# Performance work log

Hardware: AMD Instinct MI355X
Metric: run time of the kernel (lower is better)

The kernel has to match this reference:

```python
import jax, jax.numpy as jnp
import numpy as np

B, D, H = 64, 1024, 1024  # batch, input_dim, hidden_dim


def setup_inputs() -> dict:
    key = jax.random.key(0)
    k_x, k_inW, k_hW = jax.random.split(key, 3)
    # Observed binary inputs in {0,1} -> Bernoulli-sample branch never taken.
    x = jax.random.randint(k_x, (B, D), 0, 2).astype(jnp.float32)
    # Kaiming-normal init: std = sqrt(2 / fan_in)
    in_W = jax.random.normal(k_inW, (H, D), dtype=jnp.float32) * np.float32(np.sqrt(2.0 / D))
    in_b = jnp.zeros((H,), dtype=jnp.float32)
    h_W = jax.random.normal(k_hW, (D, H), dtype=jnp.float32) * np.float32(np.sqrt(2.0 / H))
    h_b = jnp.zeros((D,), dtype=jnp.float32)
    return {"x": x, "in_W": in_W, "in_b": in_b, "h_W": h_W, "h_b": h_b}


def reference(x, in_W, in_b, h_W, h_b):
    # NADE recurrence: a_i = in_b + sum_{j<i} x_j * in_W[:, j]
    # Vectorized via exclusive cumulative sum of rank-1 contributions.
    contrib = jnp.einsum("bd,hd->bdh", x, in_W)          # [B, D, H]
    cum = jnp.cumsum(contrib, axis=1)
    a = jnp.concatenate([jnp.zeros_like(cum[:, :1]), cum[:, :-1]], axis=1) + in_b  # exclusive
    h = jax.nn.relu(a)                                    # [B, D, H]
    # p_i = sigmoid(relu(a_i) . h_W[i] + h_b[i])
    p_hat = jax.nn.sigmoid(jnp.einsum("bdh,dh->bd", h, h_W) + h_b)  # [B, D]
    return p_hat
```

## Files before the change

kernel.cpp:

```cpp
#include <hip/hip_runtime.h>
#include <hip/hip_bf16.h>

#define B 64
#define D 1024
#define H 1024
#define C 32
#define L (D / C)
#define BG 4
#define NBG (B / BG)
#define HQ 4
#define HP (H / HQ)

__device__ __forceinline__ float dpp_xor1(float v) {
    int i = __builtin_bit_cast(int, v);
    i = __builtin_amdgcn_mov_dpp(i, 0xB1, 0xF, 0xF, true);
    return __builtin_bit_cast(float, i);
}
__device__ __forceinline__ float dpp_xor2(float v) {
    int i = __builtin_bit_cast(int, v);
    i = __builtin_amdgcn_mov_dpp(i, 0x4E, 0xF, 0xF, true);
    return __builtin_bit_cast(float, i);
}

__global__ void k_transpose(const float* __restrict__ in, float* __restrict__ out) {
    __shared__ float tile[32][33];
    int bx = blockIdx.x * 32;
    int by = blockIdx.y * 32;
    int tx = threadIdx.x;
    int ty = threadIdx.y;
    #pragma unroll
    for (int r = 0; r < 32; r += 8)
        tile[ty + r][tx] = in[(by + ty + r) * D + (bx + tx)];
    __syncthreads();
    #pragma unroll
    for (int r = 0; r < 32; r += 8)
        out[(bx + ty + r) * H + (by + tx)] = tile[tx][ty + r];
}

__global__ void __launch_bounds__(256)
k_chunk_sums(const float* __restrict__ x,
             const float* __restrict__ Wt,
             float* __restrict__ S) {
    int blk = blockIdx.x;
    int bg  = blk >> 7;
    int chq = blk & 127;
    int c   = chq >> 2;
    int hq  = chq & 3;
    int b0  = bg * BG;
    int tid = threadIdx.x;
    int h   = hq * HP + tid;

    __shared__ float4 xs4[L];
    if (tid < L) {
        int i = c * L + tid;
        xs4[tid] = make_float4(x[(size_t)b0 * D + i],
                               x[(size_t)(b0 + 1) * D + i],
                               x[(size_t)(b0 + 2) * D + i],
                               x[(size_t)(b0 + 3) * D + i]);
    }
    __syncthreads();

    float acc0 = 0.f, acc1 = 0.f, acc2 = 0.f, acc3 = 0.f;
    #pragma unroll
    for (int j = 0; j < L; ++j) {
        float w = Wt[(size_t)(c * L + j) * H + h];
        float4 xf = xs4[j];
        acc0 = fmaf(xf.x, w, acc0);
        acc1 = fmaf(xf.y, w, acc1);
        acc2 = fmaf(xf.z, w, acc2);
        acc3 = fmaf(xf.w, w, acc3);
    }
    S[((size_t)b0 * C + c) * H + h]       = acc0;
    S[((size_t)(b0 + 1) * C + c) * H + h] = acc1;
    S[((size_t)(b0 + 2) * C + c) * H + h] = acc2;
    S[((size_t)(b0 + 3) * C + c) * H + h] = acc3;
}

__global__ void k_scan(float* __restrict__ S) {
    int tid = blockIdx.x * blockDim.x + threadIdx.x;
    if (tid >= B * H) return;
    int b = tid / H;
    int h = tid % H;
    float run = 0.f;
    #pragma unroll
    for (int c = 0; c < C; ++c) {
        int idx = (b * C + c) * H + h;
        float v = S[idx];
        S[idx] = run;
        run += v;
    }
}

__global__ void __launch_bounds__(256)
k_nade_main(const float* __restrict__ x,
            const float* __restrict__ Wt,
            const float* __restrict__ in_b,
            const float* __restrict__ h_W,
            const float* __restrict__ h_b,
            const float* __restrict__ P,
            float* __restrict__ Q) {
    int blk = blockIdx.x;
    int bg  = blk >> 7;
    int chq = blk & 127;
    int c   = chq >> 2;
    int hq  = chq & 3;
    int b0  = bg * BG;
    int tid = threadIdx.x;
    int h   = hq * HP + tid;
    int lane = tid & 63;
    int wv = tid >> 6;
    int ph = lane & 3;

    __shared__ float4 xs4[L];
    if (tid < L) {
        int i = c * L + tid;
        xs4[tid] = make_float4(x[(size_t)b0 * D + i],
                               x[(size_t)(b0 + 1) * D + i],
                               x[(size_t)(b0 + 2) * D + i],
                               x[(size_t)(b0 + 3) * D + i]);
    }

    float ib = in_b[h];
    float a0 = P[((size_t)b0 * C + c) * H + h] + ib;
    float a1 = P[((size_t)(b0 + 1) * C + c) * H + h] + ib;
    float a2 = P[((size_t)(b0 + 2) * C + c) * H + h] + ib;
    float a3 = P[((size_t)(b0 + 3) * C + c) * H + h] + ib;

    __syncthreads();

    bool k0 = (ph == 0), k1 = (ph == 1), k2 = (ph == 2), k3 = (ph == 3);

    float pr0[8], pr1[8], pr2[8], pr3[8];
    #pragma unroll
    for (int s = 0; s < 8; ++s) { pr0[s] = 0.f; pr1[s] = 0.f; pr2[s] = 0.f; pr3[s] = 0.f; }

    #pragma unroll
    for (int il = 0; il < L; ++il) {
        int i = c * L + il;
        float w  = h_W[(size_t)i * H + h];
        float wt = Wt[(size_t)i * H + h];
        float4 xf = xs4[il];
        int s = il >> 2;
        bool keep = (il & 3) == 0 ? k0 : ((il & 3) == 1 ? k1 : ((il & 3) == 2 ? k2 : k3));

        float p0 = fmaxf(a0, 0.f) * w;
        float t0 = p0 + dpp_xor1(p0); t0 = t0 + dpp_xor2(t0);
        pr0[s] = keep ? t0 : pr0[s];
        a0 = fmaf(xf.x, wt, a0);

        float p1 = fmaxf(a1, 0.f) * w;
        float t1 = p1 + dpp_xor1(p1); t1 = t1 + dpp_xor2(t1);
        pr1[s] = keep ? t1 : pr1[s];
        a1 = fmaf(xf.y, wt, a1);

        float p2 = fmaxf(a2, 0.f) * w;
        float t2 = p2 + dpp_xor1(p2); t2 = t2 + dpp_xor2(t2);
        pr2[s] = keep ? t2 : pr2[s];
        a2 = fmaf(xf.z, wt, a2);

        float p3 = fmaxf(a3, 0.f) * w;
        float t3 = p3 + dpp_xor1(p3); t3 = t3 + dpp_xor2(t3);
        pr3[s] = keep ? t3 : pr3[s];
        a3 = fmaf(xf.w, wt, a3);
    }

    #pragma unroll
    for (int s = 0; s < 8; ++s) {
        float v;
        v = pr0[s];
        v += __shfl_xor(v, 4, 64); v += __shfl_xor(v, 8, 64);
        v += __shfl_xor(v, 16, 64); v += __shfl_xor(v, 32, 64);
        pr0[s] = v;
        v = pr1[s];
        v += __shfl_xor(v, 4, 64); v += __shfl_xor(v, 8, 64);
        v += __shfl_xor(v, 16, 64); v += __shfl_xor(v, 32, 64);
        pr1[s] = v;
        v = pr2[s];
        v += __shfl_xor(v, 4, 64); v += __shfl_xor(v, 8, 64);
        v += __shfl_xor(v, 16, 64); v += __shfl_xor(v, 32, 64);
        pr2[s] = v;
        v = pr3[s];
        v += __shfl_xor(v, 4, 64); v += __shfl_xor(v, 8, 64);
        v += __shfl_xor(v, 16, 64); v += __shfl_xor(v, 32, 64);
        pr3[s] = v;
    }

    __shared__ float red[4][BG][L];
    if (lane < 4) {
        #pragma unroll
        for (int s = 0; s < 8; ++s) {
            red[wv][0][s * 4 + lane] = pr0[s];
            red[wv][1][s * 4 + lane] = pr1[s];
            red[wv][2][s * 4 + lane] = pr2[s];
            red[wv][3][s * 4 + lane] = pr3[s];
        }
    }
    __syncthreads();

    if (tid < BG * L) {
        int b = tid >> 5;
        int il = tid & 31;
        float t = red[0][b][il] + red[1][b][il] + red[2][b][il] + red[3][b][il];
        Q[((size_t)hq * B + (b0 + b)) * D + c * L + il] = t;
    }
}

__global__ void __launch_bounds__(256)
k_combine(const float* __restrict__ Q,
          const float* __restrict__ h_b,
          float* __restrict__ out) {
    int idx = blockIdx.x * blockDim.x + threadIdx.x;
    if (idx >= B * D) return;
    int d = idx & (D - 1);
    float t = Q[idx] + Q[(size_t)B * D + idx] + Q[2 * (size_t)B * D + idx]
            + Q[3 * (size_t)B * D + idx] + h_b[d];
    out[idx] = 1.0f / (1.0f + expf(-t));
}

extern "C" void kernel_launch(void* const* d_in, const int* in_sizes, int n_in,
                              void* d_out, int out_size, void* d_ws, size_t ws_size,
                              hipStream_t stream) {
    const float* x    = (const float*)d_in[0];
    const float* in_W = (const float*)d_in[1];
    const float* in_b = (const float*)d_in[2];
    const float* h_W  = (const float*)d_in[3];
    const float* h_b  = (const float*)d_in[4];
    float* out = (float*)d_out;

    float* Wt = (float*)d_ws;
    float* S  = Wt + (size_t)D * H;
    float* Q  = S + (size_t)B * C * H;

    dim3 tb(32, 8);
    dim3 tg(D / 32, H / 32);
    k_transpose<<<tg, tb, 0, stream>>>(in_W, Wt);

    k_chunk_sums<<<NBG * C * HQ, 256, 0, stream>>>(x, Wt, S);

    k_scan<<<(B * H + 255) / 256, 256, 0, stream>>>(S);

    k_nade_main<<<NBG * C * HQ, 256, 0, stream>>>(x, Wt, in_b, h_W, h_b, S, Q);

    k_combine<<<(B * D + 255) / 256, 256, 0, stream>>>(Q, h_b, out);
}
```

Baseline: 41.20 us.

## Drop transpose and scan kernels; read in_W rows directly and prefix-sum inline

Removes the in_W transpose kernel: each thread now loads its own contiguous 32-float row segment of in_W with float4 loads into registers, in both the chunk-sum and main kernels. Removes the separate scan kernel by having the main kernel sum the preceding chunk sums itself, which costs a variable-length loop of up to 31 iterations per thread. Adds a launch_bounds occupancy hint. Two kernel launches and a full transpose pass go away, in exchange for uncoalesced strided row loads (each lane reads a different row) and redundant prefix work per block.

```diff
diff --git a/kernel.cpp b/kernel.cpp
--- a/kernel.cpp
+++ b/kernel.cpp
@@ -22,24 +22,9 @@
     return __builtin_bit_cast(float, i);
 }
 
-__global__ void k_transpose(const float* __restrict__ in, float* __restrict__ out) {
-    __shared__ float tile[32][33];
-    int bx = blockIdx.x * 32;
-    int by = blockIdx.y * 32;
-    int tx = threadIdx.x;
-    int ty = threadIdx.y;
-    #pragma unroll
-    for (int r = 0; r < 32; r += 8)
-        tile[ty + r][tx] = in[(by + ty + r) * D + (bx + tx)];
-    __syncthreads();
-    #pragma unroll
-    for (int r = 0; r < 32; r += 8)
-        out[(bx + ty + r) * H + (by + tx)] = tile[tx][ty + r];
-}
-
 __global__ void __launch_bounds__(256)
 k_chunk_sums(const float* __restrict__ x,
-             const float* __restrict__ Wt,
+             const float* __restrict__ in_W,
              float* __restrict__ S) {
     int blk = blockIdx.x;
     int bg  = blk >> 7;
@@ -58,13 +43,21 @@
                                x[(size_t)(b0 + 2) * D + i],
                                x[(size_t)(b0 + 3) * D + i]);
     }
+
+    const float* wrow = &in_W[(size_t)h * D + c * L];
+    float wr[L];
+    #pragma unroll
+    for (int q = 0; q < L / 4; ++q)
+        *reinterpret_cast<float4*>(&wr[q * 4]) =
+            *reinterpret_cast<const float4*>(wrow + q * 4);
+
     __syncthreads();
 
     float acc0 = 0.f, acc1 = 0.f, acc2 = 0.f, acc3 = 0.f;
     #pragma unroll
     for (int j = 0; j < L; ++j) {
-        float w = Wt[(size_t)(c * L + j) * H + h];
         float4 xf = xs4[j];
+        float w = wr[j];
         acc0 = fmaf(xf.x, w, acc0);
         acc1 = fmaf(xf.y, w, acc1);
         acc2 = fmaf(xf.z, w, acc2);
@@ -76,28 +69,12 @@
     S[((size_t)(b0 + 3) * C + c) * H + h] = acc3;
 }
 
-__global__ void k_scan(float* __restrict__ S) {
-    int tid = blockIdx.x * blockDim.x + threadIdx.x;
-    if (tid >= B * H) return;
-    int b = tid / H;
-    int h = tid % H;
-    float run = 0.f;
-    #pragma unroll
-    for (int c = 0; c < C; ++c) {
-        int idx = (b * C + c) * H + h;
-        float v = S[idx];
-        S[idx] = run;
-        run += v;
-    }
-}
-
-__global__ void __launch_bounds__(256)
+__global__ void __launch_bounds__(256, 2)
 k_nade_main(const float* __restrict__ x,
-            const float* __restrict__ Wt,
+            const float* __restrict__ in_W,
             const float* __restrict__ in_b,
             const float* __restrict__ h_W,
-            const float* __restrict__ h_b,
-            const float* __restrict__ P,
+            const float* __restrict__ S,
             float* __restrict__ Q) {
     int blk = blockIdx.x;
     int bg  = blk >> 7;
@@ -120,11 +97,21 @@
                                x[(size_t)(b0 + 3) * D + i]);
     }
 
+    const float* wrow = &in_W[(size_t)h * D + c * L];
+    float wr[L];
+    #pragma unroll
+    for (int q = 0; q < L / 4; ++q)
+        *reinterpret_cast<float4*>(&wr[q * 4]) =
+            *reinterpret_cast<const float4*>(wrow + q * 4);
+
     float ib = in_b[h];
-    float a0 = P[((size_t)b0 * C + c) * H + h] + ib;
-    float a1 = P[((size_t)(b0 + 1) * C + c) * H + h] + ib;
-    float a2 = P[((size_t)(b0 + 2) * C + c) * H + h] + ib;
-    float a3 = P[((size_t)(b0 + 3) * C + c) * H + h] + ib;
+    float a0 = ib, a1 = ib, a2 = ib, a3 = ib;
+    for (int cc = 0; cc < c; ++cc) {
+        a0 += S[((size_t)b0 * C + cc) * H + h];
+        a1 += S[((size_t)(b0 + 1) * C + cc) * H + h];
+        a2 += S[((size_t)(b0 + 2) * C + cc) * H + h];
+        a3 += S[((size_t)(b0 + 3) * C + cc) * H + h];
+    }
 
     __syncthreads();
 
@@ -138,7 +125,7 @@
     for (int il = 0; il < L; ++il) {
         int i = c * L + il;
         float w  = h_W[(size_t)i * H + h];
-        float wt = Wt[(size_t)i * H + h];
+        float wt = wr[il];
         float4 xf = xs4[il];
         int s = il >> 2;
         bool keep = (il & 3) == 0 ? k0 : ((il & 3) == 1 ? k1 : ((il & 3) == 2 ? k2 : k3));
@@ -227,19 +214,12 @@
     const float* h_b  = (const float*)d_in[4];
     float* out = (float*)d_out;
 
-    float* Wt = (float*)d_ws;
-    float* S  = Wt + (size_t)D * H;
-    float* Q  = S + (size_t)B * C * H;
-
-    dim3 tb(32, 8);
-    dim3 tg(D / 32, H / 32);
-    k_transpose<<<tg, tb, 0, stream>>>(in_W, Wt);
-
-    k_chunk_sums<<<NBG * C * HQ, 256, 0, stream>>>(x, Wt, S);
-
-    k_scan<<<(B * H + 255) / 256, 256, 0, stream>>>(S);
-
-    k_nade_main<<<NBG * C * HQ, 256, 0, stream>>>(x, Wt, in_b, h_W, h_b, S, Q);
+    float* S = (float*)d_ws;
+    float* Q = S + (size_t)B * C * H;
+
+    k_chunk_sums<<<NBG * C * HQ, 256, 0, stream>>>(x, in_W, S);
+
+    k_nade_main<<<NBG * C * HQ, 256, 0, stream>>>(x, in_W, in_b, h_W, S, Q);
 
     k_combine<<<(B * D + 255) / 256, 256, 0, stream>>>(Q, h_b, out);
 }
```

Measured after the change: 48.62 us. 18.0% more time.

## Fuse chunk prefix scan into main kernel, reverse chunk order for load balance

Applied to the files above, without the earlier changes.

Drops the separate scan kernel: each main-kernel block now computes its own exclusive prefix by summing the chunk sums of all earlier chunks. Chunk index is reversed so blocks with the longest prefix loops are dispatched first, balancing the uneven work. This saves one kernel launch and the scan's read-write pass. In exchange the prefix reads become redundant across blocks, roughly doubling reads of S on average.

```diff
diff --git a/kernel.cpp b/kernel.cpp
--- a/kernel.cpp
+++ b/kernel.cpp
@@ -76,33 +76,17 @@
     S[((size_t)(b0 + 3) * C + c) * H + h] = acc3;
 }
 
-__global__ void k_scan(float* __restrict__ S) {
-    int tid = blockIdx.x * blockDim.x + threadIdx.x;
-    if (tid >= B * H) return;
-    int b = tid / H;
-    int h = tid % H;
-    float run = 0.f;
-    #pragma unroll
-    for (int c = 0; c < C; ++c) {
-        int idx = (b * C + c) * H + h;
-        float v = S[idx];
-        S[idx] = run;
-        run += v;
-    }
-}
-
 __global__ void __launch_bounds__(256)
 k_nade_main(const float* __restrict__ x,
             const float* __restrict__ Wt,
             const float* __restrict__ in_b,
             const float* __restrict__ h_W,
-            const float* __restrict__ h_b,
-            const float* __restrict__ P,
+            const float* __restrict__ S,
             float* __restrict__ Q) {
     int blk = blockIdx.x;
     int bg  = blk >> 7;
     int chq = blk & 127;
-    int c   = chq >> 2;
+    int c   = (C - 1) - (chq >> 2);
     int hq  = chq & 3;
     int b0  = bg * BG;
     int tid = threadIdx.x;
@@ -112,6 +96,7 @@
     int ph = lane & 3;
 
     __shared__ float4 xs4[L];
+    __shared__ float red[4][BG][L];
     if (tid < L) {
         int i = c * L + tid;
         xs4[tid] = make_float4(x[(size_t)b0 * D + i],
@@ -121,10 +106,14 @@
     }
 
     float ib = in_b[h];
-    float a0 = P[((size_t)b0 * C + c) * H + h] + ib;
-    float a1 = P[((size_t)(b0 + 1) * C + c) * H + h] + ib;
-    float a2 = P[((size_t)(b0 + 2) * C + c) * H + h] + ib;
-    float a3 = P[((size_t)(b0 + 3) * C + c) * H + h] + ib;
+    float a0 = ib, a1 = ib, a2 = ib, a3 = ib;
+    #pragma unroll 4
+    for (int cc = 0; cc < c; ++cc) {
+        a0 += S[((size_t)b0 * C + cc) * H + h];
+        a1 += S[((size_t)(b0 + 1) * C + cc) * H + h];
+        a2 += S[((size_t)(b0 + 2) * C + cc) * H + h];
+        a3 += S[((size_t)(b0 + 3) * C + cc) * H + h];
+    }
 
     __syncthreads();
 
@@ -185,7 +174,6 @@
         pr3[s] = v;
     }
 
-    __shared__ float red[4][BG][L];
     if (lane < 4) {
         #pragma unroll
         for (int s = 0; s < 8; ++s) {
@@ -237,9 +225,7 @@
 
     k_chunk_sums<<<NBG * C * HQ, 256, 0, stream>>>(x, Wt, S);
 
-    k_scan<<<(B * H + 255) / 256, 256, 0, stream>>>(S);
-
-    k_nade_main<<<NBG * C * HQ, 256, 0, stream>>>(x, Wt, in_b, h_W, h_b, S, Q);
+    k_nade_main<<<NBG * C * HQ, 256, 0, stream>>>(x, Wt, in_b, h_W, S, Q);
 
     k_combine<<<(B * D + 255) / 256, 256, 0, stream>>>(Q, h_b, out);
 }
```

After: 43.58 us. 5.8% more time.
